# Kernel tuning notes

Measured on AMD Instinct MI355X. Metric: run time of the kernel, lower is better.

## Reference

```python
import jax, jax.numpy as jnp
import numpy as np

D_MODEL = 512
NUM_HEADS = 8
D_K = D_MODEL // NUM_HEADS
SCALE = float(np.sqrt(D_K))


def setup_inputs() -> dict:
    key = jax.random.key(0)
    ks = jax.random.split(key, 11)
    B, S, D = 2, 4096, D_MODEL
    std = 1.0 / np.sqrt(D)
    return {
        "query": jax.random.normal(ks[0], (B, S, D), jnp.float32),
        "key": jax.random.normal(ks[1], (B, S, D), jnp.float32),
        "value": jax.random.normal(ks[2], (B, S, D), jnp.float32),
        "w_q": jax.random.normal(ks[3], (D, D), jnp.float32) * std,
        "b_q": jax.random.normal(ks[4], (D,), jnp.float32) * std,
        "w_k": jax.random.normal(ks[5], (D, D), jnp.float32) * std,
        "b_k": jax.random.normal(ks[6], (D,), jnp.float32) * std,
        "w_v": jax.random.normal(ks[7], (D, D), jnp.float32) * std,
        "b_v": jax.random.normal(ks[8], (D,), jnp.float32) * std,
        "w_o": jax.random.normal(ks[9], (D, D), jnp.float32) * std,
        "b_o": jax.random.normal(ks[10], (D,), jnp.float32) * std,
    }


def reference(query, key, value, w_q, b_q, w_k, b_k, w_v, b_v, w_o, b_o):
    B, S, D = query.shape
    H, Dk = NUM_HEADS, D_K
    # Linear projections (torch Linear: x @ W^T + b), split into heads -> [B,H,S,Dk]
    Q = (query @ w_q.T + b_q).reshape(B, S, H, Dk).transpose(0, 2, 1, 3)
    K = (key @ w_k.T + b_k).reshape(B, S, H, Dk).transpose(0, 2, 1, 3)
    V = (value @ w_v.T + b_v).reshape(B, S, H, Dk).transpose(0, 2, 1, 3)
    # [B,H,S,S] attention scores — intentionally materialized like the original
    scores = jnp.einsum("bhqd,bhkd->bhqk", Q, K) / SCALE
    attn = jax.nn.softmax(scores, axis=-1)  # dropout rate 0 in eval baseline
    attended = jnp.einsum("bhqk,bhkd->bhqd", attn, V)
    attended = attended.transpose(0, 2, 1, 3).reshape(B, S, D)
    return attended @ w_o.T + b_o
```

## Files before the change

### kernel.cpp

```cpp
#include <hip/hip_runtime.h>
#include <math.h>

#define D_MODEL 512
#define NHEADS 8
#define DK 64
#define BATCH 2
#define SEQ 4096
#define NIT 32
#define ATTN_SCALE 0.18033688011112043f

typedef _Float16 half8 __attribute__((ext_vector_type(8)));
typedef _Float16 half4 __attribute__((ext_vector_type(4)));
typedef __fp16 pkhalf2 __attribute__((ext_vector_type(2)));
typedef float f32x4 __attribute__((ext_vector_type(4)));
typedef float f32x16 __attribute__((ext_vector_type(16)));

union Pk8 { _Float16 h[8]; uint4 u; };
union Pk4 { _Float16 h[4]; uint2 u; };
union Pkz { pkhalf2 h2[2]; uint2 u; };
union Un4 { uint2 u; _Float16 h[4]; };
union PFu { unsigned int u[4]; half8 h8; };

#if __has_builtin(__builtin_amdgcn_exp2f)
#define EXP2F __builtin_amdgcn_exp2f
#else
#define EXP2F exp2f
#endif

#define MFMA16(a, b, c) __builtin_amdgcn_mfma_f32_16x16x32_f16((a), (b), (c), 0, 0, 0)
#define MFMA32(a, b, c) __builtin_amdgcn_mfma_f32_32x32x16_f16((a), (b), (c), 0, 0, 0)

#define PLSWAP(x, y) asm volatile("v_permlane32_swap_b32 %0, %1" : "+v"(x), "+v"(y))

__device__ __forceinline__ unsigned int cvtpk(float a, float b) {
    union { pkhalf2 h; unsigned int u; } u_;
    u_.h = __builtin_amdgcn_cvt_pkrtz(a, b);
    return u_.u;
}

__device__ __forceinline__ void gload_lds16(const _Float16* g, _Float16* l) {
    __builtin_amdgcn_global_load_lds(
        (const __attribute__((address_space(1))) void*)g,
        (__attribute__((address_space(3))) void*)l, 16, 0, 0);
}

#define ABLK 4096
#define WBLK 256
__global__ __launch_bounds__(256)
void prep(const float* __restrict__ aq, const float* __restrict__ ak,
          const float* __restrict__ av,
          const float* __restrict__ wq, const float* __restrict__ wk,
          const float* __restrict__ wv, const float* __restrict__ wo,
          _Float16* __restrict__ dq, _Float16* __restrict__ dk,
          _Float16* __restrict__ dv,
          _Float16* __restrict__ hq, _Float16* __restrict__ hk,
          _Float16* __restrict__ hv, _Float16* __restrict__ ho) {
    int gid = blockIdx.x;
    const float* src;
    _Float16* hi;
    if (gid < 3 * ABLK) {
        const int w = gid / ABLK;
        gid -= w * ABLK;
        src = w == 0 ? aq : (w == 1 ? ak : av);
        hi  = w == 0 ? dq : (w == 1 ? dk : dv);
    } else {
        int g = gid - 3 * ABLK;
        const int w = g / WBLK;
        gid = g - w * WBLK;
        src = w == 0 ? wq : (w == 1 ? wk : (w == 2 ? wv : wo));
        hi  = w == 0 ? hq : (w == 1 ? hk : (w == 2 ? hv : ho));
    }
    const int i = (gid * 256 + threadIdx.x) * 4;
    float4 v = *(const float4*)(src + i);
    Pkz h;
    h.h2[0] = __builtin_amdgcn_cvt_pkrtz(v.x, v.y);
    h.h2[1] = __builtin_amdgcn_cvt_pkrtz(v.z, v.w);
    *(uint2*)(hi + i) = h.u;
}

__global__ __launch_bounds__(256)
void gemm_qkv(const _Float16* __restrict__ Aq, const _Float16* __restrict__ Ak,
              const _Float16* __restrict__ Av,
              const _Float16* __restrict__ Whq, const _Float16* __restrict__ Whk,
              const _Float16* __restrict__ Whv,
              const float* __restrict__ bq, const float* __restrict__ bk,
              const float* __restrict__ bv,
              _Float16* __restrict__ Qf, _Float16* __restrict__ Kf,
              _Float16* __restrict__ Vtf) {
    const int z = blockIdx.z;
    const _Float16* A    = z == 0 ? Aq  : (z == 1 ? Ak  : Av);
    const _Float16* Wh   = z == 0 ? Whq : (z == 1 ? Whk : Whv);
    const float*    bias = z == 0 ? bq  : (z == 1 ? bk  : bv);

    __shared__ __align__(16) _Float16 sA[2][128 * 64];
    __shared__ __align__(16) _Float16 sW[2][128 * 64];

    const int t    = threadIdx.x;
    const int lane = t & 63, wave = t >> 6;
    const int col  = lane & 15, quad = lane >> 4;
    const int wm   = (wave & 1) * 64, wn = (wave >> 1) * 64;
    const int m0   = blockIdx.y * 128, n0 = blockIdx.x * 128;

    const int subrow = lane >> 3;
    const int schunk = ((lane & 7) ^ subrow) * 8;

    #define STAGE_AW(K0, BUF)                                                        \
        do {                                                                          \
            _Pragma("unroll")                                                         \
            for (int j = 0; j < 4; ++j) {                                             \
                const int rw = wave * 32 + j * 8;                                     \
                gload_lds16(A  + (size_t)(m0 + rw + subrow) * 512 + (K0) + schunk,    \
                            &sA[BUF][rw * 64]);                                       \
                gload_lds16(Wh + (size_t)(n0 + rw + subrow) * 512 + (K0) + schunk,    \
                            &sW[BUF][rw * 64]);                                       \
            }                                                                         \
        } while (0)

    f32x4 acc[4][4] = {};

    STAGE_AW(0, 0);
    for (int ck = 0; ck < 8; ++ck) {
        const int cur = ck & 1;
        __syncthreads();
        if (ck + 1 < 8) STAGE_AW((ck + 1) * 64, cur ^ 1);

        #pragma unroll
        for (int kc = 0; kc < 2; ++kc) {
            const int pos = ((kc * 4 + quad) ^ (col & 7)) * 8;
            half8 af[4], wf[4];
            #pragma unroll
            for (int mt = 0; mt < 4; ++mt)
                af[mt] = *(const half8*)&sA[cur][(wm + mt * 16 + col) * 64 + pos];
            #pragma unroll
            for (int nt = 0; nt < 4; ++nt)
                wf[nt] = *(const half8*)&sW[cur][(wn + nt * 16 + col) * 64 + pos];
            #pragma unroll
            for (int mt = 0; mt < 4; ++mt)
                #pragma unroll
                for (int nt = 0; nt < 4; ++nt)
                    acc[mt][nt] = MFMA16(af[mt], wf[nt], acc[mt][nt]);
        }
    }

    float bv4[4];
    #pragma unroll
    for (int nt = 0; nt < 4; ++nt) bv4[nt] = bias[n0 + wn + nt * 16 + col];

    if (z < 2) {
        _Float16* Out = z == 0 ? Qf : Kf;
        const float alpha = z == 0 ? ATTN_SCALE : 1.0f;
        #pragma unroll
        for (int mt = 0; mt < 4; ++mt) {
            const int m = m0 + wm + mt * 16 + quad * 4;
            #pragma unroll
            for (int nt = 0; nt < 4; ++nt) {
                const int n = n0 + wn + nt * 16 + col;
                #pragma unroll
                for (int r = 0; r < 4; ++r)
                    Out[(size_t)(m + r) * 512 + n] = (_Float16)((acc[mt][nt][r] + bv4[nt]) * alpha);
            }
        }
    } else {
        #pragma unroll
        for (int mt = 0; mt < 4; ++mt) {
            const int m = m0 + wm + mt * 16 + quad * 4;
            const int b = m >> 12, s = m & (SEQ - 1);
            #pragma unroll
            for (int nt = 0; nt < 4; ++nt) {
                const int n = n0 + wn + nt * 16 + col;
                const int hh = n >> 6, d = n & (DK - 1);
                Pk4 p;
                #pragma unroll
                for (int r = 0; r < 4; ++r)
                    p.h[r] = (_Float16)(acc[mt][nt][r] + bv4[nt]);
                *(uint2*)&Vtf[((size_t)((b * NHEADS + hh) * DK + d)) * SEQ + s] = p.u;
            }
        }
    }
}

__global__ __launch_bounds__(256, 4)
void attn_mfma(const _Float16* __restrict__ Qf, const _Float16* __restrict__ Kf,
               const _Float16* __restrict__ Vtf,
               _Float16* __restrict__ Op0, _Float16* __restrict__ Op1,
               float2* __restrict__ Ml) {
    __shared__ __align__(16) _Float16 sK[2][64 * 64];
    __shared__ __align__(16) _Float16 sV[2][64 * 64];

    const int t    = threadIdx.x;
    const int lane = t & 63;
    const int wave = t >> 6;
    const int l31  = lane & 31;
    const int g    = lane >> 5;

    const int strm = blockIdx.x;
    const int h  = strm & (NHEADS - 1);
    const int z  = strm >> 3;
    const int b  = z >> 1;
    const int sp = z & 1;
    const int q0 = blockIdx.y * 128;
    const int kBase = sp * (SEQ / 2);

    const size_t rowBase = (size_t)b * SEQ;
    const size_t vBase   = ((size_t)(b * NHEADS + h)) * DK * SEQ;

    const int subrow = lane >> 3;
    const int schunk = ((lane & 7) ^ subrow) * 8;
    const _Float16* kP[2];
    const _Float16* vP[2];
    #pragma unroll
    for (int j = 0; j < 2; ++j) {
        const int rw = wave * 16 + j * 8;
        kP[j] = Kf + (rowBase + kBase + rw + subrow) * 512 + h * 64 + schunk;
        vP[j] = Vtf + vBase + (size_t)(rw + subrow) * SEQ + kBase + schunk;
        gload_lds16(kP[j], &sK[0][rw * 64]);
        gload_lds16(vP[j], &sV[0][rw * 64]);
        kP[j] += 64 * 512;
        vP[j] += 64;
    }

    half8 qf[4];
    #pragma unroll
    for (int kc = 0; kc < 4; ++kc)
        qf[kc] = *(const half8*)(Qf + (rowBase + q0 + wave * 32 + l31) * 512 +
                                 h * 64 + kc * 16 + g * 8);

    const int rs = l31 & 7;

    float m_r = 0.0f;
    float l_r = 0.0f;
    f32x16 of[2] = {};

    for (int itp = 0; itp < NIT; itp += 2) {
        #pragma unroll
        for (int cur = 0; cur < 2; ++cur) {
            const int it = itp + cur;
            __syncthreads();
            if (it + 1 < NIT) {
                #pragma unroll
                for (int j = 0; j < 2; ++j) {
                    const int rw = wave * 16 + j * 8;
                    gload_lds16(kP[j], &sK[cur ^ 1][rw * 64]);
                    gload_lds16(vP[j], &sV[cur ^ 1][rw * 64]);
                    kP[j] += 64 * 512;
                    vP[j] += 64;
                }
            }

            const float nm = -m_r;
            f32x16 nb;
            #pragma unroll
            for (int j2 = 0; j2 < 16; ++j2) nb[j2] = nm;

            f32x16 sf0, sf1;
            __builtin_amdgcn_s_setprio(1);
            #pragma unroll
            for (int kc = 0; kc < 4; ++kc) {
                const int pos = ((kc * 2 + g) ^ rs) * 8;
                half8 k0 = *(const half8*)&sK[cur][l31 * 64 + pos];
                half8 k1 = *(const half8*)&sK[cur][(32 + l31) * 64 + pos];
                sf0 = MFMA32(k0, qf[kc], kc == 0 ? nb : sf0);
                sf1 = MFMA32(k1, qf[kc], kc == 0 ? nb : sf1);
            }
            __builtin_amdgcn_s_setprio(0);

            if (it == 0) {
                float mx = sf0[0];
                #pragma unroll
                for (int j2 = 1; j2 < 16; ++j2) mx = fmaxf(mx, sf0[j2]);
                #pragma unroll
                for (int j2 = 0; j2 < 16; ++j2) mx = fmaxf(mx, sf1[j2]);
                mx = fmaxf(mx, __shfl_xor(mx, 32));
                m_r = mx;
                #pragma unroll
                for (int j2 = 0; j2 < 16; ++j2) { sf0[j2] -= mx; sf1[j2] -= mx; }
            }

            float lrs = 0.0f;
            #pragma unroll
            for (int j2 = 0; j2 < 16; ++j2) { sf0[j2] = EXP2F(sf0[j2]); lrs += sf0[j2]; }
            #pragma unroll
            for (int j2 = 0; j2 < 16; ++j2) { sf1[j2] = EXP2F(sf1[j2]); lrs += sf1[j2]; }

            PFu pf[4];
            #define MKPF(P, O)                                                   \
                do {                                                             \
                    unsigned int x1 = cvtpk(P[0], P[1]),  x2 = cvtpk(P[2], P[3]);\
                    unsigned int y1 = cvtpk(P[4], P[5]),  y2 = cvtpk(P[6], P[7]);\
                    PLSWAP(x1, y1); PLSWAP(x2, y2);                              \
                    pf[O].u[0] = x1; pf[O].u[1] = x2;                            \
                    pf[O].u[2] = y1; pf[O].u[3] = y2;                            \
                    unsigned int a1 = cvtpk(P[8], P[9]),  a2 = cvtpk(P[10], P[11]);\
                    unsigned int b1 = cvtpk(P[12], P[13]), b2 = cvtpk(P[14], P[15]);\
                    PLSWAP(a1, b1); PLSWAP(a2, b2);                              \
                    pf[O + 1].u[0] = a1; pf[O + 1].u[1] = a2;                    \
                    pf[O + 1].u[2] = b1; pf[O + 1].u[3] = b2;                    \
                } while (0)
            MKPF(sf0, 0);
            MKPF(sf1, 2);
            #undef MKPF

            __builtin_amdgcn_s_setprio(1);
            #pragma unroll
            for (int ks = 0; ks < 4; ++ks) {
                const int pos = ((ks * 2 + g) ^ rs) * 8;
                half8 v0 = *(const half8*)&sV[cur][l31 * 64 + pos];
                half8 v1 = *(const half8*)&sV[cur][(32 + l31) * 64 + pos];
                of[0] = MFMA32(v0, pf[ks].h8, of[0]);
                of[1] = MFMA32(v1, pf[ks].h8, of[1]);
            }
            __builtin_amdgcn_s_setprio(0);

            l_r += lrs;

            if (__any(lrs > 1024.0f)) {
                float pmax = sf0[0];
                #pragma unroll
                for (int j2 = 1; j2 < 16; ++j2) pmax = fmaxf(pmax, sf0[j2]);
                #pragma unroll
                for (int j2 = 0; j2 < 16; ++j2) pmax = fmaxf(pmax, sf1[j2]);
                pmax = fmaxf(pmax, __shfl_xor(pmax, 32));
                if (pmax > 1.0f) {
                    const float al = 1.0f / pmax;
                    l_r *= al;
                    #pragma unroll
                    for (int dt = 0; dt < 2; ++dt)
                        #pragma unroll
                        for (int j2 = 0; j2 < 16; ++j2)
                            of[dt][j2] *= al;
                    m_r += __log2f(pmax);
                }
            }
        }
    }

    float l = l_r + __shfl_xor(l_r, 32);
    const float inv = 1.0f / l;
    const int q = q0 + wave * 32 + l31;
    const size_t R = rowBase + q;
    _Float16* Opx = sp ? Op1 : Op0;
    #pragma unroll
    for (int dt = 0; dt < 2; ++dt) {
        #pragma unroll
        for (int m4 = 0; m4 < 4; ++m4) {
            const int d0 = dt * 32 + 8 * m4 + 4 * g;
            Pkz z2;
            z2.h2[0] = __builtin_amdgcn_cvt_pkrtz(of[dt][4 * m4 + 0] * inv,
                                                  of[dt][4 * m4 + 1] * inv);
            z2.h2[1] = __builtin_amdgcn_cvt_pkrtz(of[dt][4 * m4 + 2] * inv,
                                                  of[dt][4 * m4 + 3] * inv);
            *(uint2*)(Opx + R * 512 + h * 64 + d0) = z2.u;
        }
    }
    if (lane < 32)
        Ml[(size_t)(sp * BATCH * SEQ) * NHEADS + R * NHEADS + h] = make_float2(m_r, l);
}

__global__ __launch_bounds__(256)
void attn_merge(const _Float16* __restrict__ Op0, const _Float16* __restrict__ Op1,
                const float2* __restrict__ Ml, _Float16* __restrict__ Oh) {
    const int i4 = (blockIdx.x * 256 + threadIdx.x) * 4;
    const int R = i4 >> 9;
    const int c = i4 & 511;
    const int h = c >> 6;

    const float2 ml1 = Ml[(size_t)R * NHEADS + h];
    const float2 ml2 = Ml[(size_t)(BATCH * SEQ) * NHEADS + (size_t)R * NHEADS + h];
    const float m = fmaxf(ml1.x, ml2.x);
    float w1 = EXP2F(ml1.x - m) * ml1.y;
    float w2 = EXP2F(ml2.x - m) * ml2.y;
    const float inv = 1.0f / (w1 + w2);
    w1 *= inv; w2 *= inv;

    Un4 a, bb;
    a.u  = *(const uint2*)(Op0 + (size_t)R * 512 + c);
    bb.u = *(const uint2*)(Op1 + (size_t)R * 512 + c);

    Pkz hh;
    hh.h2[0] = __builtin_amdgcn_cvt_pkrtz(w1 * (float)a.h[0] + w2 * (float)bb.h[0],
                                          w1 * (float)a.h[1] + w2 * (float)bb.h[1]);
    hh.h2[1] = __builtin_amdgcn_cvt_pkrtz(w1 * (float)a.h[2] + w2 * (float)bb.h[2],
                                          w1 * (float)a.h[3] + w2 * (float)bb.h[3]);
    *(uint2*)(Oh + (size_t)R * 512 + c) = hh.u;
}

__global__ __launch_bounds__(256)
void gemm_out(const _Float16* __restrict__ Ah, const _Float16* __restrict__ Wh,
              const float* __restrict__ bias, float* __restrict__ C) {
    __shared__ __align__(16) _Float16 sAh[2][128 * 64];
    __shared__ __align__(16) _Float16 sWh[2][64 * 64];

    const int t    = threadIdx.x;
    const int lane = t & 63, wave = t >> 6;
    const int col  = lane & 15, quad = lane >> 4;
    const int wm   = (wave & 1) * 64, wn = (wave >> 1) * 32;
    const int m0   = blockIdx.y * 128, n0 = blockIdx.x * 64;

    const int subrow = lane >> 3;
    const int schunk = ((lane & 7) ^ subrow) * 8;

    #define STAGE_OUT(K0, BUF)                                                       \
        do {                                                                          \
            _Pragma("unroll")                                                         \
            for (int j = 0; j < 4; ++j) {                                             \
                const int rw = wave * 32 + j * 8;                                     \
                gload_lds16(Ah + (size_t)(m0 + rw + subrow) * 512 + (K0) + schunk,    \
                            &sAh[BUF][rw * 64]);                                      \
            }                                                                         \
            _Pragma("unroll")                                                         \
            for (int j = 0; j < 2; ++j) {                                             \
                const int rw = wave * 16 + j * 8;                                     \
                gload_lds16(Wh + (size_t)(n0 + rw + subrow) * 512 + (K0) + schunk,    \
                            &sWh[BUF][rw * 64]);                                      \
            }                                                                         \
        } while (0)

    f32x4 acc[4][2] = {};

    STAGE_OUT(0, 0);
    for (int ck = 0; ck < 8; ++ck) {
        const int cur = ck & 1;
        __syncthreads();
        if (ck + 1 < 8) STAGE_OUT((ck + 1) * 64, cur ^ 1);

        #pragma unroll
        for (int kc = 0; kc < 2; ++kc) {
            const int pos = ((kc * 4 + quad) ^ (col & 7)) * 8;
            half8 ahf[4], whf[2];
            #pragma unroll
            for (int mt = 0; mt < 4; ++mt)
                ahf[mt] = *(const half8*)&sAh[cur][(wm + mt * 16 + col) * 64 + pos];
            #pragma unroll
            for (int nt = 0; nt < 2; ++nt)
                whf[nt] = *(const half8*)&sWh[cur][(wn + nt * 16 + col) * 64 + pos];
            #pragma unroll
            for (int mt = 0; mt < 4; ++mt)
                #pragma unroll
                for (int nt = 0; nt < 2; ++nt)
                    acc[mt][nt] = MFMA16(ahf[mt], whf[nt], acc[mt][nt]);
        }
    }

    float bv2[2];
    #pragma unroll
    for (int nt = 0; nt < 2; ++nt) bv2[nt] = bias[n0 + wn + nt * 16 + col];

    #pragma unroll
    for (int mt = 0; mt < 4; ++mt) {
        const int m = m0 + wm + mt * 16 + quad * 4;
        #pragma unroll
        for (int nt = 0; nt < 2; ++nt) {
            const int n = n0 + wn + nt * 16 + col;
            #pragma unroll
            for (int r = 0; r < 4; ++r)
                C[(size_t)(m + r) * 512 + n] = acc[mt][nt][r] + bv2[nt];
        }
    }
}

extern "C" void kernel_launch(void* const* d_in, const int* in_sizes, int n_in,
                              void* d_out, int out_size, void* d_ws, size_t ws_size,
                              hipStream_t stream) {
    const float* query = (const float*)d_in[0];
    const float* key   = (const float*)d_in[1];
    const float* value = (const float*)d_in[2];
    const float* w_q   = (const float*)d_in[3];
    const float* b_q   = (const float*)d_in[4];
    const float* w_k   = (const float*)d_in[5];
    const float* b_k   = (const float*)d_in[6];
    const float* w_v   = (const float*)d_in[7];
    const float* b_v   = (const float*)d_in[8];
    const float* w_o   = (const float*)d_in[9];
    const float* b_o   = (const float*)d_in[10];
    float* out = (float*)d_out;

    const int WN = D_MODEL * D_MODEL;
    const size_t plane = (size_t)BATCH * SEQ * D_MODEL;

    _Float16* base = (_Float16*)d_ws;
    _Float16* Aq16 = base;
    _Float16* Ak16 = Aq16 + plane;
    _Float16* Av16 = Ak16 + plane;
    _Float16* whq  = Av16 + plane;
    _Float16* whk  = whq + WN;
    _Float16* whv  = whk + WN;
    _Float16* who  = whv + WN;
    _Float16* Qf   = who + WN;
    _Float16* Kf   = Qf + plane;
    _Float16* Vtf  = Kf + plane;
    _Float16* Op1  = Vtf + plane;
    float2*   Ml   = (float2*)(Op1 + plane);
    _Float16* Oh   = Aq16;
    _Float16* Op0  = Av16;

    dim3 blk(256);

    hipLaunchKernelGGL(prep, dim3(3 * ABLK + 4 * WBLK), blk, 0, stream,
                       query, key, value, w_q, w_k, w_v, w_o,
                       Aq16, Ak16, Av16, whq, whk, whv, who);

    hipLaunchKernelGGL(gemm_qkv, dim3(D_MODEL / 128, BATCH * SEQ / 128, 3), blk, 0, stream,
                       Aq16, Ak16, Av16,
                       whq, whk, whv,
                       b_q, b_k, b_v, Qf, Kf, Vtf);

    hipLaunchKernelGGL(attn_mfma, dim3(NHEADS * BATCH * 2, SEQ / 128), blk, 0, stream,
                       Qf, Kf, Vtf, Op0, Op1, Ml);

    hipLaunchKernelGGL(attn_merge, dim3(BATCH * SEQ * D_MODEL / 4 / 256), blk, 0, stream,
                       Op0, Op1, Ml, Oh);

    hipLaunchKernelGGL(gemm_out, dim3(D_MODEL / 64, BATCH * SEQ / 128), blk, 0, stream,
                       Oh, who, b_o, out);
}
```

Measured before the change: 239.8 us.

## Process two query tiles per wave and compute softmax row sums via MFMA

```diff
diff --git a/kernel.cpp b/kernel.cpp
--- a/kernel.cpp
+++ b/kernel.cpp
@@ -179,7 +179,7 @@
     }
 }
 
-__global__ __launch_bounds__(256, 4)
+__global__ __launch_bounds__(256, 2)
 void attn_mfma(const _Float16* __restrict__ Qf, const _Float16* __restrict__ Kf,
                const _Float16* __restrict__ Vtf,
                _Float16* __restrict__ Op0, _Float16* __restrict__ Op1,
@@ -198,7 +198,7 @@
     const int z  = strm >> 3;
     const int b  = z >> 1;
     const int sp = z & 1;
-    const int q0 = blockIdx.y * 128;
+    const int q0 = blockIdx.y * 256;
     const int kBase = sp * (SEQ / 2);
 
     const size_t rowBase = (size_t)b * SEQ;
@@ -219,17 +219,23 @@
         vP[j] += 64;
     }
 
-    half8 qf[4];
+    half8 qf[2][4];
     #pragma unroll
-    for (int kc = 0; kc < 4; ++kc)
-        qf[kc] = *(const half8*)(Qf + (rowBase + q0 + wave * 32 + l31) * 512 +
-                                 h * 64 + kc * 16 + g * 8);
+    for (int qt = 0; qt < 2; ++qt)
+        #pragma unroll
+        for (int kc = 0; kc < 4; ++kc)
+            qf[qt][kc] = *(const half8*)(Qf +
+                (rowBase + q0 + wave * 64 + qt * 32 + l31) * 512 +
+                h * 64 + kc * 16 + g * 8);
 
     const int rs = l31 & 7;
 
+    const half8 ones = {1, 1, 1, 1, 1, 1, 1, 1};
+
     float m_r = 0.0f;
-    float l_r = 0.0f;
-    f32x16 of[2] = {};
+    f32x16 nbv = {};
+    f32x16 of[2][2] = {};
+    f32x16 ofl[2] = {};
 
     for (int itp = 0; itp < NIT; itp += 2) {
         #pragma unroll
@@ -247,113 +253,101 @@
                 }
             }
 
-            const float nm = -m_r;
-            f32x16 nb;
-            #pragma unroll
-            for (int j2 = 0; j2 < 16; ++j2) nb[j2] = nm;
-
-            f32x16 sf0, sf1;
-            __builtin_amdgcn_s_setprio(1);
-            #pragma unroll
-            for (int kc = 0; kc < 4; ++kc) {
-                const int pos = ((kc * 2 + g) ^ rs) * 8;
-                half8 k0 = *(const half8*)&sK[cur][l31 * 64 + pos];
-                half8 k1 = *(const half8*)&sK[cur][(32 + l31) * 64 + pos];
-                sf0 = MFMA32(k0, qf[kc], kc == 0 ? nb : sf0);
-                sf1 = MFMA32(k1, qf[kc], kc == 0 ? nb : sf1);
+            #pragma unroll
+            for (int kt = 0; kt < 2; ++kt) {
+                f32x16 sf0, sf1;
+                __builtin_amdgcn_s_setprio(1);
+                #pragma unroll
+                for (int kc = 0; kc < 4; ++kc) {
+                    const int pos = ((kc * 2 + g) ^ rs) * 8;
+                    half8 kf = *(const half8*)&sK[cur][(kt * 32 + l31) * 64 + pos];
+                    sf0 = MFMA32(kf, qf[0][kc], kc == 0 ? nbv : sf0);
+                    sf1 = MFMA32(kf, qf[1][kc], kc == 0 ? nbv : sf1);
+                }
+                __builtin_amdgcn_s_setprio(0);
+
+                #pragma unroll
+                for (int j2 = 0; j2 < 16; ++j2) {
+                    sf0[j2] = EXP2F(sf0[j2]);
+                    sf1[j2] = EXP2F(sf1[j2]);
+                }
+
+                PFu pf0[2], pf1[2];
+                #define MKPF(P, PF)                                                  \
+                    do {                                                             \
+                        unsigned int x1 = cvtpk(P[0], P[1]),  x2 = cvtpk(P[2], P[3]);\
+                        unsigned int y1 = cvtpk(P[4], P[5]),  y2 = cvtpk(P[6], P[7]);\
+                        PLSWAP(x1, y1); PLSWAP(x2, y2);                              \
+                        PF[0].u[0] = x1; PF[0].u[1] = x2;                            \
+                        PF[0].u[2] = y1; PF[0].u[3] = y2;                            \
+                        unsigned int a1 = cvtpk(P[8], P[9]),  a2 = cvtpk(P[10], P[11]);\
+                        unsigned int b1 = cvtpk(P[12], P[13]), b2 = cvtpk(P[14], P[15]);\
+                        PLSWAP(a1, b1); PLSWAP(a2, b2);                              \
+                        PF[1].u[0] = a1; PF[1].u[1] = a2;                            \
+                        PF[1].u[2] = b1; PF[1].u[3] = b2;                            \
+                    } while (0)
+                MKPF(sf0, pf0);
+                MKPF(sf1, pf1);
+                #undef MKPF
+
+                __builtin_amdgcn_s_setprio(1);
+                #pragma unroll
+                for (int ks2 = 0; ks2 < 2; ++ks2) {
+                    const int ks = kt * 2 + ks2;
+                    const int pos = ((ks * 2 + g) ^ rs) * 8;
+                    half8 v0 = *(const half8*)&sV[cur][l31 * 64 + pos];
+                    half8 v1 = *(const half8*)&sV[cur][(32 + l31) * 64 + pos];
+                    of[0][0] = MFMA32(v0, pf0[ks2].h8, of[0][0]);
+                    of[0][1] = MFMA32(v1, pf0[ks2].h8, of[0][1]);
+                    of[1][0] = MFMA32(v0, pf1[ks2].h8, of[1][0]);
+                    of[1][1] = MFMA32(v1, pf1[ks2].h8, of[1][1]);
+                    ofl[0] = MFMA32(ones, pf0[ks2].h8, ofl[0]);
+                    ofl[1] = MFMA32(ones, pf1[ks2].h8, ofl[1]);
+                }
+                __builtin_amdgcn_s_setprio(0);
             }
-            __builtin_amdgcn_s_setprio(0);
-
-            if (it == 0) {
-                float mx = sf0[0];
-                #pragma unroll
-                for (int j2 = 1; j2 < 16; ++j2) mx = fmaxf(mx, sf0[j2]);
-                #pragma unroll
-                for (int j2 = 0; j2 < 16; ++j2) mx = fmaxf(mx, sf1[j2]);
-                mx = fmaxf(mx, __shfl_xor(mx, 32));
-                m_r = mx;
-                #pragma unroll
-                for (int j2 = 0; j2 < 16; ++j2) { sf0[j2] -= mx; sf1[j2] -= mx; }
+
+            if (__any(fmaxf(ofl[0][0], ofl[1][0]) > 1048576.0f)) {
+                const float al = 0.0009765625f;
+                #pragma unroll
+                for (int qt = 0; qt < 2; ++qt) {
+                    #pragma unroll
+                    for (int j2 = 0; j2 < 16; ++j2) {
+                        of[qt][0][j2] *= al;
+                        of[qt][1][j2] *= al;
+                        ofl[qt][j2]   *= al;
+                    }
+                }
+                m_r += 10.0f;
+                #pragma unroll
+                for (int j2 = 0; j2 < 16; ++j2) nbv[j2] = -m_r;
             }
-
-            float lrs = 0.0f;
-            #pragma unroll
-            for (int j2 = 0; j2 < 16; ++j2) { sf0[j2] = EXP2F(sf0[j2]); lrs += sf0[j2]; }
-            #pragma unroll
-            for (int j2 = 0; j2 < 16; ++j2) { sf1[j2] = EXP2F(sf1[j2]); lrs += sf1[j2]; }
-
-            PFu pf[4];
-            #define MKPF(P, O)                                                   \
-                do {                                                             \
-                    unsigned int x1 = cvtpk(P[0], P[1]),  x2 = cvtpk(P[2], P[3]);\
-                    unsigned int y1 = cvtpk(P[4], P[5]),  y2 = cvtpk(P[6], P[7]);\
-                    PLSWAP(x1, y1); PLSWAP(x2, y2);                              \
-                    pf[O].u[0] = x1; pf[O].u[1] = x2;                            \
-                    pf[O].u[2] = y1; pf[O].u[3] = y2;                            \
-                    unsigned int a1 = cvtpk(P[8], P[9]),  a2 = cvtpk(P[10], P[11]);\
-                    unsigned int b1 = cvtpk(P[12], P[13]), b2 = cvtpk(P[14], P[15]);\
-                    PLSWAP(a1, b1); PLSWAP(a2, b2);                              \
-                    pf[O + 1].u[0] = a1; pf[O + 1].u[1] = a2;                    \
-                    pf[O + 1].u[2] = b1; pf[O + 1].u[3] = b2;                    \
-                } while (0)
-            MKPF(sf0, 0);
-            MKPF(sf1, 2);
-            #undef MKPF
-
-            __builtin_amdgcn_s_setprio(1);
-            #pragma unroll
-            for (int ks = 0; ks < 4; ++ks) {
-                const int pos = ((ks * 2 + g) ^ rs) * 8;
-                half8 v0 = *(const half8*)&sV[cur][l31 * 64 + pos];
-                half8 v1 = *(const half8*)&sV[cur][(32 + l31) * 64 + pos];
-                of[0] = MFMA32(v0, pf[ks].h8, of[0]);
-                of[1] = MFMA32(v1, pf[ks].h8, of[1]);
-            }
-            __builtin_amdgcn_s_setprio(0);
-
-            l_r += lrs;
-
-            if (__any(lrs > 1024.0f)) {
-                float pmax = sf0[0];
-                #pragma unroll
-                for (int j2 = 1; j2 < 16; ++j2) pmax = fmaxf(pmax, sf0[j2]);
-                #pragma unroll
-                for (int j2 = 0; j2 < 16; ++j2) pmax = fmaxf(pmax, sf1[j2]);
-                pmax = fmaxf(pmax, __shfl_xor(pmax, 32));
-                if (pmax > 1.0f) {
-                    const float al = 1.0f / pmax;
-                    l_r *= al;
-                    #pragma unroll
-                    for (int dt = 0; dt < 2; ++dt)
-                        #pragma unroll
-                        for (int j2 = 0; j2 < 16; ++j2)
-                            of[dt][j2] *= al;
-                    m_r += __log2f(pmax);
-                }
-            }
-        }
-    }
-
-    float l = l_r + __shfl_xor(l_r, 32);
-    const float inv = 1.0f / l;
-    const int q = q0 + wave * 32 + l31;
-    const size_t R = rowBase + q;
+        }
+    }
+
     _Float16* Opx = sp ? Op1 : Op0;
     #pragma unroll
-    for (int dt = 0; dt < 2; ++dt) {
-        #pragma unroll
-        for (int m4 = 0; m4 < 4; ++m4) {
-            const int d0 = dt * 32 + 8 * m4 + 4 * g;
-            Pkz z2;
-            z2.h2[0] = __builtin_amdgcn_cvt_pkrtz(of[dt][4 * m4 + 0] * inv,
-                                                  of[dt][4 * m4 + 1] * inv);
-            z2.h2[1] = __builtin_amdgcn_cvt_pkrtz(of[dt][4 * m4 + 2] * inv,
-                                                  of[dt][4 * m4 + 3] * inv);
-            *(uint2*)(Opx + R * 512 + h * 64 + d0) = z2.u;
-        }
-    }
-    if (lane < 32)
-        Ml[(size_t)(sp * BATCH * SEQ) * NHEADS + R * NHEADS + h] = make_float2(m_r, l);
+    for (int qt = 0; qt < 2; ++qt) {
+        const float l = ofl[qt][0];
+        const float inv = 1.0f / l;
+        const int q = q0 + wave * 64 + qt * 32 + l31;
+        const size_t R = rowBase + q;
+        #pragma unroll
+        for (int dt = 0; dt < 2; ++dt) {
+            #pragma unroll
+            for (int m4 = 0; m4 < 4; ++m4) {
+                const int d0 = dt * 32 + 8 * m4 + 4 * g;
+                Pkz z2;
+                z2.h2[0] = __builtin_amdgcn_cvt_pkrtz(of[qt][dt][4 * m4 + 0] * inv,
+                                                      of[qt][dt][4 * m4 + 1] * inv);
+                z2.h2[1] = __builtin_amdgcn_cvt_pkrtz(of[qt][dt][4 * m4 + 2] * inv,
+                                                      of[qt][dt][4 * m4 + 3] * inv);
+                *(uint2*)(Opx + R * 512 + h * 64 + d0) = z2.u;
+            }
+        }
+        if (lane < 32)
+            Ml[(size_t)(sp * BATCH * SEQ) * NHEADS + R * NHEADS + h] = make_float2(m_r, l);
+    }
 }
 
 __global__ __launch_bounds__(256)
@@ -504,7 +498,7 @@
                        whq, whk, whv,
                        b_q, b_k, b_v, Qf, Kf, Vtf);
 
-    hipLaunchKernelGGL(attn_mfma, dim3(NHEADS * BATCH * 2, SEQ / 128), blk, 0, stream,
+    hipLaunchKernelGGL(attn_mfma, dim3(NHEADS * BATCH * 2, SEQ / 256), blk, 0, stream,
                        Qf, Kf, Vtf, Op0, Op1, Ml);
 
     hipLaunchKernelGGL(attn_merge, dim3(BATCH * SEQ * D_MODEL / 4 / 256), blk, 0, stream,
```

Result: no change. 239.3 us (-0.2%).
